# Kernel optimization log

Measured on AMD Instinct MI355X. Metric: run time of the kernel, lower is better.

Reference implementation:

```python
import jax, jax.numpy as jnp
import numpy as np

B, K, G, C = 64, 4000, 200, 91
LAMBDA_BOX, LAMBDA_CLS, LAMBDA_OBJ = 5.0, 1.0, 1.0
EPS = 1e-9


def _make_boxes(key, lead_shape):
    k1, k2 = jax.random.split(key)
    tl = jax.random.uniform(k1, lead_shape + (2,)) * 0.7
    wh = jax.random.uniform(k2, lead_shape + (2,)) * 0.29 + 0.01
    return jnp.concatenate([tl, tl + wh], axis=-1)


def setup_inputs() -> dict:
    key = jax.random.key(0)
    ks = jax.random.split(key, 6)
    pred_boxes = _make_boxes(ks[0], (B, K))
    pred_obj_logits = jax.random.normal(ks[1], (B, K), dtype=jnp.float32)
    pred_cls_logits = jax.random.normal(ks[2], (B, K, C), dtype=jnp.float32)
    gt_boxes = _make_boxes(ks[3], (B, G))
    gt_labels = jax.random.randint(ks[4], (B, G), 0, C)
    n_gt = jax.random.randint(ks[5], (B,), 1, G + 1)
    gt_mask = jnp.arange(G)[None, :] < n_gt[:, None]
    return dict(pred_boxes=pred_boxes, pred_obj_logits=pred_obj_logits,
                pred_cls_logits=pred_cls_logits, gt_boxes=gt_boxes,
                gt_labels=gt_labels, gt_mask=gt_mask)


def _area(x):
    return jnp.clip(x[..., 2] - x[..., 0], 0.0) * jnp.clip(x[..., 3] - x[..., 1], 0.0)


def _pairwise_iou(a, b):
    # a: (K,4), b: (G,4) -> (K,G)
    tl = jnp.maximum(a[:, None, :2], b[None, :, :2])
    br = jnp.minimum(a[:, None, 2:], b[None, :, 2:])
    wh = jnp.clip(br - tl, 0.0)
    inter = wh[..., 0] * wh[..., 1]
    union = jnp.clip(_area(a)[:, None] + _area(b)[None, :] - inter, EPS)
    return inter / union


def _ciou_loss(pb, gb):
    # pb, gb: (M,4) matched pairs; elementwise CIoU loss = 1 - CIoU
    tl = jnp.maximum(pb[:, :2], gb[:, :2])
    br = jnp.minimum(pb[:, 2:], gb[:, 2:])
    wh = jnp.clip(br - tl, 0.0)
    inter = wh[:, 0] * wh[:, 1]
    iou = inter / jnp.clip(_area(pb) + _area(gb) - inter, EPS)
    px = (pb[:, 0] + pb[:, 2]) * 0.5
    py = (pb[:, 1] + pb[:, 3]) * 0.5
    tx = (gb[:, 0] + gb[:, 2]) * 0.5
    ty = (gb[:, 1] + gb[:, 3]) * 0.5
    rho2 = (px - tx) ** 2 + (py - ty) ** 2
    etl = jnp.minimum(pb[:, :2], gb[:, :2])
    ebr = jnp.maximum(pb[:, 2:], gb[:, 2:])
    c2 = jnp.clip((ebr[:, 0] - etl[:, 0]) ** 2 + (ebr[:, 1] - etl[:, 1]) ** 2, EPS)
    pw = jnp.clip(pb[:, 2] - pb[:, 0], EPS)
    ph = jnp.clip(pb[:, 3] - pb[:, 1], EPS)
    tw = jnp.clip(gb[:, 2] - gb[:, 0], EPS)
    th = jnp.clip(gb[:, 3] - gb[:, 1], EPS)
    v = (4.0 / jnp.pi ** 2) * (jnp.arctan(tw / th) - jnp.arctan(pw / ph)) ** 2
    alpha = jax.lax.stop_gradient(v / (1.0 - iou + v + EPS))  # torch.no_grad
    return 1.0 - (iou - rho2 / c2 - alpha * v)


def _greedy_match(iou0):
    # iou0: (K,G), invalid gt columns pre-masked to -1. Fixed min(K,G)-step
    # argmax-and-mask scan reproducing the torch greedy loop (break -> valid=False).
    Gd = iou0.shape[1]
    steps = min(iou0.shape[0], Gd)

    def step(m, _):
        flat = jnp.argmax(m)
        p = flat // Gd
        g = flat % Gd
        valid = m.reshape(-1)[flat] >= 0.0
        m2 = m.at[p, :].set(-1.0).at[:, g].set(-1.0)
        return jnp.where(valid, m2, m), (p, g, valid)

    _, (ps, gs, vs) = jax.lax.scan(step, iou0, None, length=steps)
    return ps, gs, vs


def _per_batch(pred_b, cls_b, gt_b, labels_b, mask_b):
    iou = jax.lax.stop_gradient(_pairwise_iou(pred_b, gt_b))  # matching is non-diff (.item() in torch)
    iou = jnp.where(mask_b[None, :], iou, -1.0)
    ps, gs, vs = _greedy_match(iou)
    vf = vs.astype(pred_b.dtype)
    n = jnp.sum(vf)
    denom = jnp.maximum(n, 1.0)
    pb = pred_b[ps]
    gb = gt_b[gs]
    lbox = jnp.sum(_ciou_loss(pb, gb) * vf) / denom
    logp = jax.nn.log_softmax(cls_b[ps], axis=-1)
    lce = -jnp.take_along_axis(logp, labels_b[gs][:, None], axis=1)[:, 0]
    lcls = jnp.sum(lce * vf) / denom
    obj_tgt = jnp.zeros((pred_b.shape[0],), pred_b.dtype).at[
        jnp.where(vs, ps, pred_b.shape[0])].set(1.0, mode='drop')
    return lbox, lcls, obj_tgt, n > 0.0


def reference(pred_boxes, pred_obj_logits, pred_cls_logits, gt_boxes, gt_labels, gt_mask):
    lbox_b, lcls_b, obj_tgt, has = jax.vmap(_per_batch)(
        pred_boxes, pred_cls_logits, gt_boxes, gt_labels, gt_mask)
    hf = has.astype(pred_boxes.dtype)
    nb = jnp.maximum(jnp.sum(hf), 1.0)
    loss_box = jnp.sum(lbox_b * hf) / nb
    loss_cls = jnp.sum(lcls_b * hf) / nb
    # BCEWithLogits(mean): softplus(x) - t*x
    loss_obj = jnp.mean(jax.nn.softplus(pred_obj_logits) - obj_tgt * pred_obj_logits)
    total = LAMBDA_BOX * loss_box + LAMBDA_CLS * loss_cls + LAMBDA_OBJ * loss_obj
    return total, loss_box, loss_cls, loss_obj
```

## Files before the change

kernel.cpp:

```cpp
#include <hip/hip_runtime.h>
#include <math.h>

#define B_ 64
#define K_ 4000
#define G_ 200
#define C_ 91
#define EPS_ 1e-9f
#define NW_ 16
#define DEPTH_ 32
typedef unsigned long long ull;

#define WS_FLAG 0
#define WS_PART 256
#define WS_TOP 327680

__device__ __forceinline__ float box_area(float4 a) {
#pragma clang fp contract(off)
  return fmaxf(a.z - a.x, 0.f) * fmaxf(a.w - a.y, 0.f);
}

__device__ __forceinline__ float iou_ab(float4 a, float aA, float4 b, float aB) {
#pragma clang fp contract(off)
  float tlx = fmaxf(a.x, b.x), tly = fmaxf(a.y, b.y);
  float brx = fminf(a.z, b.z), bry = fminf(a.w, b.w);
  float w = fmaxf(brx - tlx, 0.f), h = fmaxf(bry - tly, 0.f);
  float inter = w * h;
  float uni = fmaxf(aA + aB - inter, EPS_);
  return inter / uni;
}

__device__ __forceinline__ float ciou_loss(float4 p, float4 g) {
  float tlx = fmaxf(p.x, g.x), tly = fmaxf(p.y, g.y);
  float brx = fminf(p.z, g.z), bry = fminf(p.w, g.w);
  float w = fmaxf(brx - tlx, 0.f), h = fmaxf(bry - tly, 0.f);
  float inter = w * h;
  float areaP = fmaxf(p.z - p.x, 0.f) * fmaxf(p.w - p.y, 0.f);
  float areaG = fmaxf(g.z - g.x, 0.f) * fmaxf(g.w - g.y, 0.f);
  float iou = inter / fmaxf(areaP + areaG - inter, EPS_);
  float px = (p.x + p.z) * 0.5f, py = (p.y + p.w) * 0.5f;
  float tx = (g.x + g.z) * 0.5f, ty = (g.y + g.w) * 0.5f;
  float rho2 = (px - tx) * (px - tx) + (py - ty) * (py - ty);
  float ex = fmaxf(p.z, g.z) - fminf(p.x, g.x);
  float ey = fmaxf(p.w, g.w) - fminf(p.y, g.y);
  float c2 = fmaxf(ex * ex + ey * ey, EPS_);
  float pw = fmaxf(p.z - p.x, EPS_), ph = fmaxf(p.w - p.y, EPS_);
  float tw = fmaxf(g.z - g.x, EPS_), th = fmaxf(g.w - g.y, EPS_);
  float dat = atanf(tw / th) - atanf(pw / ph);
  float v = (4.0f / (float)(M_PI * M_PI)) * dat * dat;
  float alpha = v / ((1.f - iou) + v + EPS_);
  return 1.f - (iou - rho2 / c2 - alpha * v);
}

__global__ void kdetect(const unsigned char* m8, int* flag) {
  int b = threadIdx.x;
  int ok = 1;
  const unsigned char* r = m8 + b * G_;
  if (r[0] != 1) ok = 0;
  int seen0 = 0;
  for (int g = 0; g < G_; ++g) {
    unsigned char c = r[g];
    if (c > 1) { ok = 0; break; }
    if (c == 0) seen0 = 1;
    else if (seen0) { ok = 0; break; }
  }
  int all = __all(ok);
  if (b == 0) *flag = all ? 1 : 0;
}

__device__ __forceinline__ float block_sum(float v, float* s_red) {
  for (int off = 32; off > 0; off >>= 1) v += __shfl_xor(v, off);
  int lane = threadIdx.x & 63, wid = threadIdx.x >> 6;
  if (lane == 0) s_red[wid] = v;
  __syncthreads();
  float r = 0.f;
  if (wid == 0) {
    float t = (lane < NW_) ? s_red[lane] : 0.f;
    for (int off = 32; off > 0; off >>= 1) t += __shfl_xor(t, off);
    r = t;
  }
  __syncthreads();
  return r;
}

__device__ __forceinline__ ull wave_maxkey(ull k) {
  for (int off = 32; off > 0; off >>= 1) {
    ull o = __shfl_xor(k, off);
    if (o > k) k = o;
  }
  return k;
}

#define TOP4_INS(key, t0, t1, t2, t3)                   \
  if ((key) > t3) {                                     \
    t3 = (key);                                         \
    ull tmp_;                                           \
    if (t3 > t2) { tmp_ = t2; t2 = t3; t3 = tmp_; }     \
    if (t2 > t1) { tmp_ = t1; t1 = t2; t2 = tmp_; }     \
    if (t1 > t0) { tmp_ = t0; t0 = t1; t1 = tmp_; }     \
  }

__device__ __forceinline__ void extract_list(ull t0, ull t1, ull t2, ull t3,
                                             ull* dst, int lane) {
  int supplied = 0, written = 0;
  for (int o = 0; o < DEPTH_; ++o) {
    ull m = wave_maxkey(t0);
    if (m == 0ull) break;
    int dn = 0;
    if (t0 == m) {
      t0 = t1; t1 = t2; t2 = t3; t3 = 0;
      if (++supplied == 4) dn = 1;
    }
    if (lane == 0) dst[o] = m;
    ++written;
    if (__any(dn)) break;
  }
  for (int o = written + lane; o < DEPTH_; o += 64) dst[o] = 0ull;
}

__global__ __launch_bounds__(1024) void kinit(const float* __restrict__ pred_boxes,
                                              const float* __restrict__ gt_boxes,
                                              const void* __restrict__ gt_mask,
                                              char* __restrict__ ws) {
  __shared__ float4 s_p[K_];
  const int blk = blockIdx.x;
  const int b = blk >> 3, oct = blk & 7;
  const int tid = threadIdx.x, lane = tid & 63, wid = tid >> 6;
  const int msk8 = *(const int*)(ws + WS_FLAG);
  const float4* p4 = (const float4*)pred_boxes + (size_t)b * K_;
  const float4* g4 = (const float4*)gt_boxes + (size_t)b * G_;

  for (int i = tid; i < K_; i += 1024) s_p[i] = p4[i];
  __syncthreads();

  const int base = oct * 25;
  const int colA = base + wid;
  const int colB = base + 16 + wid;
  const bool hasB = (wid < 9);
  ull* wtop = (ull*)(ws + WS_TOP);

  int vA, vB = 0;
  if (msk8) vA = ((const unsigned char*)gt_mask)[(size_t)b * G_ + colA] != 0;
  else      vA = ((const int*)gt_mask)[(size_t)b * G_ + colA] != 0;
  if (hasB) {
    if (msk8) vB = ((const unsigned char*)gt_mask)[(size_t)b * G_ + colB] != 0;
    else      vB = ((const int*)gt_mask)[(size_t)b * G_ + colB] != 0;
  }

  float4 gbA, gbB;
  float gAA = 0.f, gAB = 0.f;
  if (vA) { gbA = g4[colA]; gAA = box_area(gbA); }
  if (vB) { gbB = g4[colB]; gAB = box_area(gbB); }

  ull a0 = 0, a1 = 0, a2 = 0, a3 = 0;
  ull b0 = 0, b1 = 0, b2 = 0, b3 = 0;
  if (vA | vB) {
#pragma unroll 2
    for (int k = lane; k < K_; k += 64) {
      float4 pb = s_p[k];
      float ar = box_area(pb);
      if (vA) {
        float iou = iou_ab(pb, ar, gbA, gAA);
        ull e = ((ull)__float_as_uint(iou) << 12) | (ull)(4095 - k);
        TOP4_INS(e, a0, a1, a2, a3);
      }
      if (vB) {
        float iou = iou_ab(pb, ar, gbB, gAB);
        ull e = ((ull)__float_as_uint(iou) << 12) | (ull)(4095 - k);
        TOP4_INS(e, b0, b1, b2, b3);
      }
    }
  }
  {
    ull* dstA = wtop + ((size_t)b * G_ + colA) * DEPTH_;
    if (vA) extract_list(a0, a1, a2, a3, dstA, lane);
    else    for (int o = lane; o < DEPTH_; o += 64) dstA[o] = 0ull;
  }
  if (hasB) {
    ull* dstB = wtop + ((size_t)b * G_ + colB) * DEPTH_;
    if (vB) extract_list(b0, b1, b2, b3, dstB, lane);
    else    for (int o = lane; o < DEPTH_; o += 64) dstB[o] = 0ull;
  }
}

__global__ __launch_bounds__(1024) void kmerged(
    const float* __restrict__ pred_boxes, const float* __restrict__ obj_logits,
    const float* __restrict__ cls_logits, const float* __restrict__ gt_boxes,
    const int* __restrict__ gt_labels, char* __restrict__ ws) {
  __shared__ float s_gx[G_], s_gy[G_], s_gz[G_], s_gw[G_], s_garea[G_];
  __shared__ unsigned char s_rowused[4096];
  __shared__ ull s_toplist[G_][DEPTH_ + 1];
  __shared__ int s_mp[G_];
  __shared__ unsigned short s_mg[G_];
  __shared__ int s_cnt;
  __shared__ float s_red[NW_];
  const int b = blockIdx.x;
  const int tid = threadIdx.x, lane = tid & 63, wid = tid >> 6;
  const float4* p4 = (const float4*)pred_boxes + (size_t)b * K_;
  const float4* g4 = (const float4*)gt_boxes + (size_t)b * G_;
  const ull* wtop = (const ull*)(ws + WS_TOP);

  for (int g = tid; g < G_; g += 1024) {
    float4 gb = g4[g];
    s_gx[g] = gb.x; s_gy[g] = gb.y; s_gz[g] = gb.z; s_gw[g] = gb.w;
    s_garea[g] = box_area(gb);
  }
  for (int k = tid; k < 4096; k += 1024) s_rowused[k] = 0;
  for (int i = tid; i < G_ * DEPTH_; i += 1024)
    s_toplist[i / DEPTH_][i % DEPTH_] = wtop[((size_t)b * G_) * DEPTH_ + i];
  __syncthreads();

  if (wid == 0) {
    ull key0 = 0, key1 = 0, key2 = 0, key3 = 0;
    int ptr0 = DEPTH_, ptr1 = DEPTH_, ptr2 = DEPTH_, ptr3 = DEPTH_;
    int cloc = 0;
#define SLOTINIT(S)                                                        \
    { int col = S * 64 + lane;                                             \
      if (col < G_) {                                                      \
        ull h_ = s_toplist[col][0];                                        \
        if (h_ != 0ull) {                                                  \
          key##S = (h_ << 8) | (ull)(255 - col); ptr##S = 1; ++cloc; } } }
    SLOTINIT(0) SLOTINIT(1) SLOTINIT(2) SLOTINIT(3)
#undef SLOTINIT
    for (int off = 32; off > 0; off >>= 1) cloc += __shfl_xor(cloc, off);
    const int cnt = cloc;
    if (lane == 0) s_cnt = cnt;

    for (int step = 0; step < cnt;) {
      ull a1 = key0, a2 = key1;
      if (key1 > key0) { a1 = key1; a2 = key0; }
      if (key2 > a1) { a2 = a1; a1 = key2; } else if (key2 > a2) a2 = key2;
      if (key3 > a1) { a2 = a1; a1 = key3; } else if (key3 > a2) a2 = key3;
      for (int off = 32; off > 0; off >>= 1) {
        ull b1 = __shfl_xor(a1, off), b2 = __shfl_xor(a2, off);
        if (b1 > a1) { a2 = (a1 > b2) ? a1 : b2; a1 = b1; }
        else { a2 = (b1 > a2) ? b1 : a2; }
      }
      const int p1 = 4095 - (int)((a1 >> 8) & 0xFFF);
      const int g1v = 255 - (int)(a1 & 0xFF);
      const int p2 = 4095 - (int)((a2 >> 8) & 0xFFF);
      const int g2v = 255 - (int)(a2 & 0xFF);
      const bool do2 = (a2 != 0ull) && (p2 != p1) && (step + 1 < cnt);
      if (lane == 0) {
        s_mp[step] = p1; s_mg[step] = (unsigned short)g1v; s_rowused[p1] = 1;
        if (do2) { s_mp[step + 1] = p2; s_mg[step + 1] = (unsigned short)g2v; s_rowused[p2] = 1; }
      }
      __builtin_amdgcn_wave_barrier();
      const int gd2 = do2 ? g2v : -1;
      const int pd2 = do2 ? p2 : -1;
      int need = 0;
#define DEMOTE(S)                                                           \
      { int col = S * 64 + lane; ull kk = key##S;                           \
        if (kk != 0ull) {                                                   \
          if (col == g1v || col == gd2) { key##S = 0ull; }                  \
          else { int krow = 4095 - (int)((kk >> 8) & 0xFFF);                \
            if (krow == p1 || krow == pd2) {                                \
              ull nk = 0ull; int np = ptr##S;                               \
              while (np < DEPTH_) {                                         \
                ull e = s_toplist[col][np]; ++np;                           \
                if (e == 0ull) { np = DEPTH_; break; }                      \
                int pr = 4095 - (int)((e >> 12) & 0xFFF);                   \
                if (!s_rowused[pr]) { nk = (e << 8) | (ull)(255 - col); break; } \
              }                                                             \
              ptr##S = np; key##S = nk;                                     \
              if (nk == 0ull) need |= (1 << S); } } } }
      DEMOTE(0) DEMOTE(1) DEMOTE(2) DEMOTE(3)
#undef DEMOTE
      while (__any(need)) {
        unsigned long long bal = __ballot(need != 0);
        int src = (int)__builtin_ctzll(bal);
        int myslot = need ? __builtin_ctz(need) : 0;
        int slot = __shfl(myslot, src);
        int col = slot * 64 + src;
        float4 gb = make_float4(s_gx[col], s_gy[col], s_gz[col], s_gw[col]);
        float gA = s_garea[col];
        ull t0 = 0, t1 = 0, t2 = 0, t3 = 0;
#pragma unroll 2
        for (int k = lane; k < K_; k += 64) {
          if (!s_rowused[k]) {
            float4 pb = p4[k];
            float iou = iou_ab(pb, box_area(pb), gb, gA);
            ull e = ((ull)__float_as_uint(iou) << 12) | (ull)(4095 - k);
            TOP4_INS(e, t0, t1, t2, t3);
          }
        }
        int r0 = 0, r1 = 0, r2 = 0, r3 = 0;
        for (int i = 0; i < 64; ++i) {
          ull o0 = __shfl(t0, i), o1 = __shfl(t1, i);
          ull o2 = __shfl(t2, i), o3 = __shfl(t3, i);
          r0 += (o0 > t0) + (o1 > t0) + (o2 > t0) + (o3 > t0);
          r1 += (o0 > t1) + (o1 > t1) + (o2 > t1) + (o3 > t1);
          r2 += (o0 > t2) + (o1 > t2) + (o2 > t2) + (o3 > t2);
          r3 += (o0 > t3) + (o1 > t3) + (o2 > t3) + (o3 > t3);
        }
        int cut = (t3 != 0ull) ? (r3 + 1) : 0x7FFFFFFF;
        int nc = (t0 != 0ull) + (t1 != 0ull) + (t2 != 0ull) + (t3 != 0ull);
        for (int off = 32; off > 0; off >>= 1) {
          int oc = __shfl_xor(cut, off);
          cut = (oc < cut) ? oc : cut;
          nc += __shfl_xor(nc, off);
        }
        const int Lf = (cut < DEPTH_) ? cut : DEPTH_;
        const int zstart = (Lf < nc) ? Lf : nc;
        if (t0 != 0ull && r0 < Lf) s_toplist[col][r0] = t0;
        if (t1 != 0ull && r1 < Lf) s_toplist[col][r1] = t1;
        if (t2 != 0ull && r2 < Lf) s_toplist[col][r2] = t2;
        if (t3 != 0ull && r3 < Lf) s_toplist[col][r3] = t3;
        for (int o = lane; o < DEPTH_; o += 64)
          if (o >= zstart) s_toplist[col][o] = 0ull;
        __builtin_amdgcn_wave_barrier();
        ull newhead = s_toplist[col][0];
        if (lane == src) {
          ull nk = (newhead << 8) | (ull)(255 - col);
          if (slot == 0) { key0 = nk; ptr0 = 1; }
          else if (slot == 1) { key1 = nk; ptr1 = 1; }
          else if (slot == 2) { key2 = nk; ptr2 = 1; }
          else { key3 = nk; ptr3 = 1; }
          need &= ~(1 << slot);
        }
        __builtin_amdgcn_wave_barrier();
      }
      step += do2 ? 2 : 1;
    }
  }
  __syncthreads();

  const int cnt = s_cnt;
  float lbox = 0.f, lcls = 0.f;
  for (int i = tid; i < cnt; i += 1024) {
    int p = s_mp[i], g = s_mg[i];
    float4 pb = p4[p];
    float4 gb = make_float4(s_gx[g], s_gy[g], s_gz[g], s_gw[g]);
    lbox += ciou_loss(pb, gb);
    int label = gt_labels[(size_t)b * G_ + g];
    const float* lg = cls_logits + ((size_t)b * K_ + p) * C_;
    float m = -1e30f;
    for (int cc = 0; cc < C_; ++cc) m = fmaxf(m, lg[cc]);
    float s = 0.f;
    for (int cc = 0; cc < C_; ++cc) s += expf(lg[cc] - m);
    lcls += (m + logf(s)) - lg[label];
  }
  float obj = 0.f;
  const float* ol = obj_logits + (size_t)b * K_;
  for (int k = tid; k < K_; k += 1024) {
    float x = ol[k];
    float sp = fmaxf(x, 0.f) + log1pf(expf(-fabsf(x)));
    if (s_rowused[k]) sp -= x;
    obj += sp;
  }
  lbox = block_sum(lbox, s_red);
  lcls = block_sum(lcls, s_red);
  obj = block_sum(obj, s_red);
  if (tid == 0) {
    float* partials = (float*)(ws + WS_PART);
    float n = (float)cnt;
    float denom = fmaxf(n, 1.f);
    partials[b * 4 + 0] = lbox / denom;
    partials[b * 4 + 1] = lcls / denom;
    partials[b * 4 + 2] = obj;
    partials[b * 4 + 3] = (n > 0.f) ? 1.f : 0.f;
  }
}

__global__ void kfinal(const char* __restrict__ ws, float* __restrict__ out) {
  int b = threadIdx.x;
  const float* partials = (const float*)(ws + WS_PART);
  float lb = partials[b * 4 + 0], lc = partials[b * 4 + 1];
  float ob = partials[b * 4 + 2], hf = partials[b * 4 + 3];
  float sb = lb * hf, sc = lc * hf, sh = hf, so = ob;
  for (int off = 32; off > 0; off >>= 1) {
    sb += __shfl_xor(sb, off);
    sc += __shfl_xor(sc, off);
    sh += __shfl_xor(sh, off);
    so += __shfl_xor(so, off);
  }
  if (b == 0) {
    float nb = fmaxf(sh, 1.f);
    float box = sb / nb, cls = sc / nb;
    float obj = so / (float)(B_ * K_);
    out[0] = 5.f * box + cls + obj;
    out[1] = box;
    out[2] = cls;
    out[3] = obj;
  }
}

extern "C" void kernel_launch(void* const* d_in, const int* in_sizes, int n_in,
                              void* d_out, int out_size, void* d_ws, size_t ws_size,
                              hipStream_t stream) {
  const float* pred_boxes = (const float*)d_in[0];
  const float* obj_logits = (const float*)d_in[1];
  const float* cls_logits = (const float*)d_in[2];
  const float* gt_boxes = (const float*)d_in[3];
  const int* gt_labels = (const int*)d_in[4];
  const void* gt_mask = d_in[5];
  float* out = (float*)d_out;
  char* ws = (char*)d_ws;

  hipLaunchKernelGGL(kdetect, dim3(1), dim3(64), 0, stream,
                     (const unsigned char*)gt_mask, (int*)(ws + WS_FLAG));
  hipLaunchKernelGGL(kinit, dim3(B_ * 8), dim3(1024), 0, stream,
                     pred_boxes, gt_boxes, gt_mask, ws);
  hipLaunchKernelGGL(kmerged, dim3(B_), dim3(1024), 0, stream,
                     pred_boxes, obj_logits, cls_logits, gt_boxes, gt_labels, ws);
  hipLaunchKernelGGL(kfinal, dim3(1), dim3(64), 0, stream, ws, out);
}
```

Before: 256.0 us.

## Accept up to four greedy matches per step via wave-wide top-4 merge

The greedy matching loop now finds the wave-wide top-4 column-head keys with a bitonic-style merge across lanes, where it previously found only the top-2. It accepts up to four matches per iteration when their rows are distinct, cutting the number of serial greedy steps. The demotion scan of each column's sorted candidate list also reads two entries per loop iteration to shorten the dependent LDS load chain. The trade-off is more shuffles per step, and the validity conditions must keep the order identical to sequential greedy matching.

```diff
diff --git a/kernel.cpp b/kernel.cpp
--- a/kernel.cpp
+++ b/kernel.cpp
@@ -90,6 +90,22 @@
   return k;
 }
 
+__device__ __forceinline__ void merge4_stage(ull& v0, ull& v1, ull& v2, ull& v3,
+                                             int off) {
+  ull w0 = __shfl_xor(v0, off), w1 = __shfl_xor(v1, off);
+  ull w2 = __shfl_xor(v2, off), w3 = __shfl_xor(v3, off);
+  ull t0 = v0 > w3 ? v0 : w3;
+  ull t1 = v1 > w2 ? v1 : w2;
+  ull t2 = v2 > w1 ? v2 : w1;
+  ull t3 = v3 > w0 ? v3 : w0;
+  ull x;
+  if (t2 > t0) { x = t0; t0 = t2; t2 = x; }
+  if (t3 > t1) { x = t1; t1 = t3; t3 = x; }
+  if (t1 > t0) { x = t0; t0 = t1; t1 = x; }
+  if (t3 > t2) { x = t2; t2 = t3; t3 = x; }
+  v0 = t0; v1 = t1; v2 = t2; v3 = t3;
+}
+
 #define TOP4_INS(key, t0, t1, t2, t3)                   \
   if ((key) > t3) {                                     \
     t3 = (key);                                         \
@@ -226,40 +242,58 @@
     if (lane == 0) s_cnt = cnt;
 
     for (int step = 0; step < cnt;) {
-      ull a1 = key0, a2 = key1;
-      if (key1 > key0) { a1 = key1; a2 = key0; }
-      if (key2 > a1) { a2 = a1; a1 = key2; } else if (key2 > a2) a2 = key2;
-      if (key3 > a1) { a2 = a1; a1 = key3; } else if (key3 > a2) a2 = key3;
-      for (int off = 32; off > 0; off >>= 1) {
-        ull b1 = __shfl_xor(a1, off), b2 = __shfl_xor(a2, off);
-        if (b1 > a1) { a2 = (a1 > b2) ? a1 : b2; a1 = b1; }
-        else { a2 = (b1 > a2) ? b1 : a2; }
-      }
-      const int p1 = 4095 - (int)((a1 >> 8) & 0xFFF);
-      const int g1v = 255 - (int)(a1 & 0xFF);
-      const int p2 = 4095 - (int)((a2 >> 8) & 0xFFF);
-      const int g2v = 255 - (int)(a2 & 0xFF);
-      const bool do2 = (a2 != 0ull) && (p2 != p1) && (step + 1 < cnt);
+      ull v0 = key0, v1 = key1, v2 = key2, v3 = key3, x;
+      if (v1 > v0) { x = v0; v0 = v1; v1 = x; }
+      if (v3 > v2) { x = v2; v2 = v3; v3 = x; }
+      if (v2 > v0) { x = v0; v0 = v2; v2 = x; }
+      if (v3 > v1) { x = v1; v1 = v3; v3 = x; }
+      if (v2 > v1) { x = v1; v1 = v2; v2 = x; }
+      merge4_stage(v0, v1, v2, v3, 32);
+      merge4_stage(v0, v1, v2, v3, 16);
+      merge4_stage(v0, v1, v2, v3, 8);
+      merge4_stage(v0, v1, v2, v3, 4);
+      merge4_stage(v0, v1, v2, v3, 2);
+      merge4_stage(v0, v1, v2, v3, 1);
+      const int P0 = 4095 - (int)((v0 >> 8) & 0xFFF), G0 = 255 - (int)(v0 & 0xFF);
+      const int P1 = 4095 - (int)((v1 >> 8) & 0xFFF), G1 = 255 - (int)(v1 & 0xFF);
+      const int P2 = 4095 - (int)((v2 >> 8) & 0xFFF), G2 = 255 - (int)(v2 & 0xFF);
+      const int P3 = 4095 - (int)((v3 >> 8) & 0xFFF), G3 = 255 - (int)(v3 & 0xFF);
+      const int lim = cnt - step;
+      const bool a2 = (v1 != 0ull) && (P1 != P0) && (lim > 1);
+      const bool a3 = a2 && (v2 != 0ull) && (P2 != P0) && (P2 != P1) && (lim > 2);
+      const bool a4 = a3 && (v3 != 0ull) && (P3 != P0) && (P3 != P1) && (P3 != P2) && (lim > 3);
+      const int nacc = 1 + (int)a2 + (int)a3 + (int)a4;
       if (lane == 0) {
-        s_mp[step] = p1; s_mg[step] = (unsigned short)g1v; s_rowused[p1] = 1;
-        if (do2) { s_mp[step + 1] = p2; s_mg[step + 1] = (unsigned short)g2v; s_rowused[p2] = 1; }
+        s_mp[step] = P0; s_mg[step] = (unsigned short)G0; s_rowused[P0] = 1;
+        if (a2) { s_mp[step + 1] = P1; s_mg[step + 1] = (unsigned short)G1; s_rowused[P1] = 1; }
+        if (a3) { s_mp[step + 2] = P2; s_mg[step + 2] = (unsigned short)G2; s_rowused[P2] = 1; }
+        if (a4) { s_mp[step + 3] = P3; s_mg[step + 3] = (unsigned short)G3; s_rowused[P3] = 1; }
       }
       __builtin_amdgcn_wave_barrier();
-      const int gd2 = do2 ? g2v : -1;
-      const int pd2 = do2 ? p2 : -1;
+      const int gA = G0, gB = a2 ? G1 : -1, gC = a3 ? G2 : -1, gD = a4 ? G3 : -1;
+      const int pA = P0, pB = a2 ? P1 : -1, pC = a3 ? P2 : -1, pD = a4 ? P3 : -1;
       int need = 0;
 #define DEMOTE(S)                                                           \
       { int col = S * 64 + lane; ull kk = key##S;                           \
         if (kk != 0ull) {                                                   \
-          if (col == g1v || col == gd2) { key##S = 0ull; }                  \
-          else { int krow = 4095 - (int)((kk >> 8) & 0xFFF);                \
-            if (krow == p1 || krow == pd2) {                                \
+          if (col == gA || col == gB || col == gC || col == gD) {           \
+            key##S = 0ull;                                                  \
+          } else {                                                          \
+            int krow = 4095 - (int)((kk >> 8) & 0xFFF);                     \
+            if (krow == pA || krow == pB || krow == pC || krow == pD) {     \
               ull nk = 0ull; int np = ptr##S;                               \
               while (np < DEPTH_) {                                         \
-                ull e = s_toplist[col][np]; ++np;                           \
-                if (e == 0ull) { np = DEPTH_; break; }                      \
-                int pr = 4095 - (int)((e >> 12) & 0xFFF);                   \
-                if (!s_rowused[pr]) { nk = (e << 8) | (ull)(255 - col); break; } \
+                ull e0 = s_toplist[col][np];                                \
+                ull e1 = (np + 1 < DEPTH_) ? s_toplist[col][np + 1] : 0ull; \
+                int pr0 = 4095 - (int)((e0 >> 12) & 0xFFF);                 \
+                int pr1 = 4095 - (int)((e1 >> 12) & 0xFFF);                 \
+                unsigned char u0 = s_rowused[pr0];                          \
+                unsigned char u1 = s_rowused[pr1];                          \
+                if (e0 == 0ull) { np = DEPTH_; break; }                     \
+                if (!u0) { nk = (e0 << 8) | (ull)(255 - col); np += 1; break; } \
+                if (e1 == 0ull) { np = DEPTH_; break; }                     \
+                if (!u1) { nk = (e1 << 8) | (ull)(255 - col); np += 2; break; } \
+                np += 2;                                                    \
               }                                                             \
               ptr##S = np; key##S = nk;                                     \
               if (nk == 0ull) need |= (1 << S); } } } }
@@ -272,13 +306,13 @@
         int slot = __shfl(myslot, src);
         int col = slot * 64 + src;
         float4 gb = make_float4(s_gx[col], s_gy[col], s_gz[col], s_gw[col]);
-        float gA = s_garea[col];
+        float gA2 = s_garea[col];
         ull t0 = 0, t1 = 0, t2 = 0, t3 = 0;
 #pragma unroll 2
         for (int k = lane; k < K_; k += 64) {
           if (!s_rowused[k]) {
             float4 pb = p4[k];
-            float iou = iou_ab(pb, box_area(pb), gb, gA);
+            float iou = iou_ab(pb, box_area(pb), gb, gA2);
             ull e = ((ull)__float_as_uint(iou) << 12) | (ull)(4095 - k);
             TOP4_INS(e, t0, t1, t2, t3);
           }
@@ -319,7 +353,7 @@
         }
         __builtin_amdgcn_wave_barrier();
       }
-      step += do2 ? 2 : 1;
+      step += nacc;
     }
   }
   __syncthreads();
```

Result: no change. 253.9 us (-0.8%).
